# Optimization experiments

Measured on AMD Instinct MI355X. Metric: run time of the kernel, lower is better.

## Reference

```python
import jax, jax.numpy as jnp
import numpy as np

N_HEADS = 4

def log_cosh(x):
    # numerically stable log(cosh(x)) = |x| + log1p(exp(-2|x|)) - log(2)
    ax = jnp.abs(x)
    return ax + jnp.log1p(jnp.exp(-2.0 * ax)) - jnp.log(2.0)

def setup_inputs() -> dict:
    key = jax.random.key(0)
    ks = jax.random.split(key, 7)
    B, I, A, E, H = 4, 2048, 2048, 256, N_HEADS
    return {
        "query": jax.random.normal(ks[0], (B, I, E), dtype=jnp.float32),
        "key": jax.random.normal(ks[1], (B, A, E), dtype=jnp.float32),
        "value": jax.random.normal(ks[2], (B, A, E), dtype=jnp.float32),
        "distances": jax.random.uniform(ks[3], (B, I, A), dtype=jnp.float32),
        "in_proj_w": jax.random.normal(ks[4], (3 * E, E), dtype=jnp.float32) * 0.05,
        "out_proj_w": jax.random.normal(ks[5], (E, E), dtype=jnp.float32) * 0.05,
        "mass_w": jax.random.normal(ks[6], (H, E), dtype=jnp.float32) * 0.05,
    }

def reference(query, key, value, distances, in_proj_w, out_proj_w, mass_w):
    B, I, E = query.shape
    A = key.shape[1]
    H = N_HEADS
    D = E // H
    # distance-decay additive bias: mass is (B, A, H), nonnegative via log_cosh
    mass = log_cosh(key @ mass_w.T)                       # (B, A, H)
    bias = jnp.einsum('bah,bia->bhia', -mass, distances)  # (B, H, I, A)
    # nn.MultiheadAttention (bias=False) projections
    wq, wk, wv = jnp.split(in_proj_w, 3, axis=0)          # each (E, E)
    q = (query @ wq.T).reshape(B, I, H, D).transpose(0, 2, 1, 3)  # (B,H,I,D)
    k = (key @ wk.T).reshape(B, A, H, D).transpose(0, 2, 1, 3)    # (B,H,A,D)
    v = (value @ wv.T).reshape(B, A, H, D).transpose(0, 2, 1, 3)  # (B,H,A,D)
    scale = 1.0 / jnp.sqrt(jnp.asarray(D, dtype=q.dtype))
    scores = jnp.einsum('bhid,bhad->bhia', q, k) * scale + bias
    attn = jax.nn.softmax(scores, axis=-1)
    o = jnp.einsum('bhia,bhad->bhid', attn, v)            # (B,H,I,D)
    o = o.transpose(0, 2, 1, 3).reshape(B, I, E)
    return o @ out_proj_w.T
```

## Files before the change

kernel.cpp:

```cpp
#include <hip/hip_runtime.h>
#include <hip/hip_bf16.h>
#include <math.h>

#define BB 4
#define II 2048
#define AA 2048
#define EE 256
#define HH 4

typedef __bf16 bf16_t;
typedef bf16_t bf16x8 __attribute__((ext_vector_type(8)));
typedef bf16_t bf16x4 __attribute__((ext_vector_type(4)));
typedef float  f32x4  __attribute__((ext_vector_type(4)));

static __device__ __forceinline__ f32x4 mfma16(bf16x8 a, bf16x8 b, f32x4 c) {
    return __builtin_amdgcn_mfma_f32_16x16x32_bf16(a, b, c, 0, 0, 0);
}

__global__ __launch_bounds__(256) void mass_kernel(
    const float* __restrict__ key, const float* __restrict__ mass_w,
    float* __restrict__ massT)
{
    const int w = threadIdx.x >> 6;
    const int l = threadIdx.x & 63;
    const int row = blockIdx.x * 4 + w;
    f32x4 kv = *(const f32x4*)(key + (size_t)row * EE + l * 4);
    const int b = row >> 11, a = row & (AA - 1);
    #pragma unroll
    for (int h = 0; h < HH; ++h) {
        f32x4 mw = *(const f32x4*)(mass_w + h * EE + l * 4);
        float s = kv[0]*mw[0] + kv[1]*mw[1] + kv[2]*mw[2] + kv[3]*mw[3];
        #pragma unroll
        for (int off = 32; off >= 1; off >>= 1) s += __shfl_xor(s, off, 64);
        if (l == 0) {
            float ax = fabsf(s);
            massT[((size_t)b * HH + h) * AA + a] =
                ax + log1pf(__expf(-2.0f * ax)) - 0.693147180559945f;
        }
    }
}

template<int TRANS>
__global__ __launch_bounds__(256) void proj_gemm(
    const float* __restrict__ Aop, const float* __restrict__ Bop,
    bf16_t* __restrict__ Cout)
{
    __shared__ __align__(16) bf16_t sA[64][72];
    __shared__ __align__(16) bf16_t sB[64][72];
    const int t = threadIdx.x;
    const int w = t >> 6, l = t & 63, g = l >> 4, q = l & 15;
    const int wm = w >> 1, wn = w & 1;
    const int m0 = blockIdx.x * 64, n0 = blockIdx.y * 64;
    const int r = t >> 2, s = t & 3;

    f32x4 acc[2][2] = {};

    for (int kt = 0; kt < 4; ++kt) {
        {
            const float* ga = Aop + (size_t)(m0 + r) * EE + kt * 64 + s * 16;
            float tmp[16];
            *(f32x4*)&tmp[0]  = *(const f32x4*)(ga + 0);
            *(f32x4*)&tmp[4]  = *(const f32x4*)(ga + 4);
            *(f32x4*)&tmp[8]  = *(const f32x4*)(ga + 8);
            *(f32x4*)&tmp[12] = *(const f32x4*)(ga + 12);
            bf16x8 w0, w1;
            #pragma unroll
            for (int i = 0; i < 8; ++i) { w0[i] = (bf16_t)tmp[i]; w1[i] = (bf16_t)tmp[8 + i]; }
            *(bf16x8*)&sA[r][s * 16]     = w0;
            *(bf16x8*)&sA[r][s * 16 + 8] = w1;
        }
        {
            const float* gb = Bop + (size_t)(n0 + r) * EE + kt * 64 + s * 16;
            float tmp[16];
            *(f32x4*)&tmp[0]  = *(const f32x4*)(gb + 0);
            *(f32x4*)&tmp[4]  = *(const f32x4*)(gb + 4);
            *(f32x4*)&tmp[8]  = *(const f32x4*)(gb + 8);
            *(f32x4*)&tmp[12] = *(const f32x4*)(gb + 12);
            bf16x8 w0, w1;
            #pragma unroll
            for (int i = 0; i < 8; ++i) { w0[i] = (bf16_t)tmp[i]; w1[i] = (bf16_t)tmp[8 + i]; }
            *(bf16x8*)&sB[r][s * 16]     = w0;
            *(bf16x8*)&sB[r][s * 16 + 8] = w1;
        }
        __syncthreads();
        #pragma unroll
        for (int ks = 0; ks < 2; ++ks) {
            bf16x8 aA[2], aB[2];
            #pragma unroll
            for (int f = 0; f < 2; ++f) {
                aA[f] = *(const bf16x8*)&sA[wm * 32 + f * 16 + q][ks * 32 + g * 8];
                aB[f] = *(const bf16x8*)&sB[wn * 32 + f * 16 + q][ks * 32 + g * 8];
            }
            #pragma unroll
            for (int fm = 0; fm < 2; ++fm)
            #pragma unroll
            for (int fn = 0; fn < 2; ++fn)
                acc[fm][fn] = mfma16(aA[fm], aB[fn], acc[fm][fn]);
        }
        __syncthreads();
    }
    #pragma unroll
    for (int fm = 0; fm < 2; ++fm)
    #pragma unroll
    for (int fn = 0; fn < 2; ++fn)
    #pragma unroll
    for (int j = 0; j < 4; ++j) {
        const int m = m0 + wm * 32 + fm * 16 + g * 4 + j;
        const int n = n0 + wn * 32 + fn * 16 + q;
        const bf16_t v = (bf16_t)acc[fm][fn][j];
        if (TRANS == 0) {
            Cout[(size_t)m * EE + n] = v;
        } else {
            const int b = n >> 11, a = n & (AA - 1);
            Cout[(size_t)b * (AA * EE) + (size_t)(a >> 6) * (EE * 64) + m * 64 + (a & 63)] = v;
        }
    }
}

__global__ __launch_bounds__(256) void out_gemm(
    const bf16_t* __restrict__ Aop, const float* __restrict__ Bop,
    float* __restrict__ Cout)
{
    __shared__ __align__(16) bf16_t sA[64][72];
    __shared__ __align__(16) bf16_t sB[64][72];
    const int t = threadIdx.x;
    const int w = t >> 6, l = t & 63, g = l >> 4, q = l & 15;
    const int wm = w >> 1, wn = w & 1;
    const int m0 = blockIdx.x * 64, n0 = blockIdx.y * 64;
    const int r = t >> 2, s = t & 3;

    f32x4 acc[2][2] = {};

    for (int kt = 0; kt < 4; ++kt) {
        {
            const bf16_t* ga = Aop + (size_t)(m0 + r) * EE + kt * 64 + s * 16;
            *(bf16x8*)&sA[r][s * 16]     = *(const bf16x8*)(ga);
            *(bf16x8*)&sA[r][s * 16 + 8] = *(const bf16x8*)(ga + 8);
        }
        {
            const float* gb = Bop + (size_t)(n0 + r) * EE + kt * 64 + s * 16;
            float tmp[16];
            *(f32x4*)&tmp[0]  = *(const f32x4*)(gb + 0);
            *(f32x4*)&tmp[4]  = *(const f32x4*)(gb + 4);
            *(f32x4*)&tmp[8]  = *(const f32x4*)(gb + 8);
            *(f32x4*)&tmp[12] = *(const f32x4*)(gb + 12);
            bf16x8 w0, w1;
            #pragma unroll
            for (int i = 0; i < 8; ++i) { w0[i] = (bf16_t)tmp[i]; w1[i] = (bf16_t)tmp[8 + i]; }
            *(bf16x8*)&sB[r][s * 16]     = w0;
            *(bf16x8*)&sB[r][s * 16 + 8] = w1;
        }
        __syncthreads();
        #pragma unroll
        for (int ks = 0; ks < 2; ++ks) {
            bf16x8 aA[2], aB[2];
            #pragma unroll
            for (int f = 0; f < 2; ++f) {
                aA[f] = *(const bf16x8*)&sA[wm * 32 + f * 16 + q][ks * 32 + g * 8];
                aB[f] = *(const bf16x8*)&sB[wn * 32 + f * 16 + q][ks * 32 + g * 8];
            }
            #pragma unroll
            for (int fm = 0; fm < 2; ++fm)
            #pragma unroll
            for (int fn = 0; fn < 2; ++fn)
                acc[fm][fn] = mfma16(aA[fm], aB[fn], acc[fm][fn]);
        }
        __syncthreads();
    }
    #pragma unroll
    for (int fm = 0; fm < 2; ++fm)
    #pragma unroll
    for (int fn = 0; fn < 2; ++fn)
    #pragma unroll
    for (int j = 0; j < 4; ++j) {
        const int m = m0 + wm * 32 + fm * 16 + g * 4 + j;
        const int n = n0 + wn * 32 + fn * 16 + q;
        Cout[(size_t)m * EE + n] = acc[fm][fn][j];
    }
}

__global__ __launch_bounds__(256, 2) void attn_kernel(
    const bf16_t* __restrict__ Qp, const bf16_t* __restrict__ Kp,
    const bf16_t* __restrict__ Vt, const float* __restrict__ massT,
    const float* __restrict__ dist, bf16_t* __restrict__ Obuf)
{
    __shared__ __align__(16) bf16_t sK[2][64 * 64];
    __shared__ __align__(16) bf16_t sV[2][64 * 64];
    __shared__ __align__(16) float  sD[2][64 * 68];
    __shared__ __align__(16) float  sM[AA];

    const int t = threadIdx.x;
    const int w = t >> 6, l = t & 63, g = l >> 4, q = l & 15;
    const int h = blockIdx.y, b = blockIdx.z;
    const int i0 = blockIdx.x * 64;

    {
        const float* gm = massT + ((size_t)b * HH + h) * AA + t * 8;
        *(f32x4*)&sM[t * 8]     = *(const f32x4*)(gm);
        *(f32x4*)&sM[t * 8 + 4] = *(const f32x4*)(gm + 4);
    }

    bf16x8 qf[2];
    #pragma unroll
    for (int ks = 0; ks < 2; ++ks)
        qf[ks] = *(const bf16x8*)(Qp + (size_t)(b * II + i0 + w * 16 + q) * EE
                                     + h * 64 + ks * 32 + g * 8);

    const int sr = t >> 2;
    const int sc = (t & 3) * 2;
    const int z0 = ((sc)     ^ (sr & 7)) * 8;
    const int z1 = ((sc + 1) ^ (sr & 7)) * 8;

    const bf16_t* gK = Kp + ((size_t)b * AA + sr) * EE + h * 64 + sc * 8;
    const bf16_t* gV = Vt + (size_t)b * (AA * EE) + (size_t)(h * 64 + sr) * 64 + sc * 8;
    const float*  gD = dist + ((size_t)b * II + i0 + sr) * AA + (t & 3) * 16;

    bf16x8 rk0, rk1, rv0, rv1;
    f32x4 rd0, rd1, rd2, rd3;

    auto load_regs = [&](int a0) {
        const bf16_t* pk = gK + (size_t)a0 * EE;
        rk0 = *(const bf16x8*)(pk);
        rk1 = *(const bf16x8*)(pk + 8);
        const bf16_t* pv = gV + (size_t)(a0 >> 6) * (EE * 64);
        rv0 = *(const bf16x8*)(pv);
        rv1 = *(const bf16x8*)(pv + 8);
        const float* pd = gD + a0;
        rd0 = *(const f32x4*)(pd);
        rd1 = *(const f32x4*)(pd + 4);
        rd2 = *(const f32x4*)(pd + 8);
        rd3 = *(const f32x4*)(pd + 12);
    };
    auto write_stage = [&](int buf) {
        *(bf16x8*)&sK[buf][sr * 64 + z0] = rk0;
        *(bf16x8*)&sK[buf][sr * 64 + z1] = rk1;
        *(bf16x8*)&sV[buf][sr * 64 + z0] = rv0;
        *(bf16x8*)&sV[buf][sr * 64 + z1] = rv1;
        float* pd = &sD[buf][sr * 68 + (t & 3) * 16];
        *(f32x4*)(pd)      = rd0;
        *(f32x4*)(pd + 4)  = rd1;
        *(f32x4*)(pd + 8)  = rd2;
        *(f32x4*)(pd + 12) = rd3;
    };

    float mrun = -INFINITY, lrun = 0.f;
    f32x4 oacc[4] = {};

    load_regs(0);
    write_stage(0);
    __syncthreads();

    for (int tt = 0; tt < 32; ++tt) {
        const int buf = tt & 1;
        const int a0 = tt * 64;
        if (tt < 31) load_regs(a0 + 64);

        f32x4 st[4] = {};
        __builtin_amdgcn_s_setprio(1);
        #pragma unroll
        for (int fa = 0; fa < 4; ++fa) {
            const int row = fa * 16 + q;
            #pragma unroll
            for (int ks = 0; ks < 2; ++ks) {
                bf16x8 ak = *(const bf16x8*)&sK[buf][row * 64 + (((ks * 4 + g) ^ (row & 7)) * 8)];
                st[fa] = mfma16(ak, qf[ks], st[fa]);
            }
        }
        __builtin_amdgcn_s_setprio(0);

        float mloc = -INFINITY;
        const int drow = w * 16 + q;
        #pragma unroll
        for (int fa = 0; fa < 4; ++fa) {
            f32x4 df = *(const f32x4*)&sD[buf][drow * 68 + fa * 16 + g * 4];
            f32x4 ms = *(const f32x4*)&sM[a0 + fa * 16 + g * 4];
            #pragma unroll
            for (int j = 0; j < 4; ++j) {
                float sv = st[fa][j] * 0.125f - ms[j] * df[j];
                st[fa][j] = sv;
                mloc = fmaxf(mloc, sv);
            }
        }
        mloc = fmaxf(mloc, __shfl_xor(mloc, 16, 64));
        mloc = fmaxf(mloc, __shfl_xor(mloc, 32, 64));

        const bool skip = __all(mloc <= mrun);
        float mnew, sc;
        if (skip) { mnew = mrun; sc = 1.f; }
        else { mnew = fmaxf(mrun, mloc); sc = __expf(mrun - mnew); mrun = mnew; }

        float rs = 0.f;
        #pragma unroll
        for (int fa = 0; fa < 4; ++fa)
        #pragma unroll
        for (int j = 0; j < 4; ++j) {
            float e = __expf(st[fa][j] - mnew);
            st[fa][j] = e;
            rs += e;
        }
        rs += __shfl_xor(rs, 16, 64);
        rs += __shfl_xor(rs, 32, 64);
        lrun = lrun * sc + rs;

        if (!skip) {
            float osc[4];
            #pragma unroll
            for (int j = 0; j < 4; ++j) osc[j] = __shfl(sc, g * 4 + j, 64);
            #pragma unroll
            for (int fd = 0; fd < 4; ++fd)
            #pragma unroll
            for (int j = 0; j < 4; ++j) oacc[fd][j] *= osc[j];
        }

        bf16x8 pa[2];
        #pragma unroll
        for (int ka = 0; ka < 2; ++ka)
        #pragma unroll
        for (int j = 0; j < 8; ++j)
            pa[ka][j] = (bf16_t)st[2 * ka + (j >> 2)][j & 3];

        __builtin_amdgcn_s_setprio(1);
        #pragma unroll
        for (int ka = 0; ka < 2; ++ka)
        #pragma unroll
        for (int fd = 0; fd < 4; ++fd) {
            const int row = fd * 16 + q;
            const int base = row * 64 + (g & 1) * 4;
            bf16x4 v0 = *(const bf16x4*)&sV[buf][base + (((ka * 4 +     (g >> 1)) ^ (row & 7)) * 8)];
            bf16x4 v1 = *(const bf16x4*)&sV[buf][base + (((ka * 4 + 2 + (g >> 1)) ^ (row & 7)) * 8)];
            bf16x8 bv;
            #pragma unroll
            for (int j = 0; j < 4; ++j) { bv[j] = v0[j]; bv[4 + j] = v1[j]; }
            oacc[fd] = mfma16(pa[ka], bv, oacc[fd]);
        }
        __builtin_amdgcn_s_setprio(0);

        if (tt < 31) write_stage(buf ^ 1);
        __syncthreads();
    }

    float inv[4];
    #pragma unroll
    for (int j = 0; j < 4; ++j) inv[j] = 1.0f / __shfl(lrun, g * 4 + j, 64);
    #pragma unroll
    for (int fd = 0; fd < 4; ++fd)
    #pragma unroll
    for (int j = 0; j < 4; ++j) {
        const int mrow = i0 + w * 16 + g * 4 + j;
        const int ncol = h * 64 + fd * 16 + q;
        Obuf[(size_t)(b * II + mrow) * EE + ncol] = (bf16_t)(oacc[fd][j] * inv[j]);
    }
}

extern "C" void kernel_launch(void* const* d_in, const int* in_sizes, int n_in,
                              void* d_out, int out_size, void* d_ws, size_t ws_size,
                              hipStream_t stream)
{
    const float* query  = (const float*)d_in[0];
    const float* key    = (const float*)d_in[1];
    const float* value  = (const float*)d_in[2];
    const float* dist   = (const float*)d_in[3];
    const float* in_w   = (const float*)d_in[4];
    const float* out_w  = (const float*)d_in[5];
    const float* mass_w = (const float*)d_in[6];
    float* out = (float*)d_out;

    char* ws = (char*)d_ws;
    bf16_t* Qp    = (bf16_t*)(ws);
    bf16_t* Kp    = (bf16_t*)(ws + 1 * 4194304);
    bf16_t* Vt    = (bf16_t*)(ws + 2 * 4194304);
    bf16_t* Obuf  = (bf16_t*)(ws + 3 * 4194304);
    float*  massT = (float*) (ws + 4 * 4194304);

    dim3 blk(256);
    proj_gemm<0><<<dim3(128, 4), blk, 0, stream>>>(query, in_w,           Qp);
    proj_gemm<0><<<dim3(128, 4), blk, 0, stream>>>(key,   in_w + 65536,   Kp);
    proj_gemm<1><<<dim3(4, 128), blk, 0, stream>>>(in_w + 131072, value,  Vt);
    mass_kernel<<<dim3(2048), blk, 0, stream>>>(key, mass_w, massT);
    attn_kernel<<<dim3(32, 4, 4), blk, 0, stream>>>(Qp, Kp, Vt, massT, dist, Obuf);
    out_gemm<<<dim3(128, 4), blk, 0, stream>>>(Obuf, out_w, out);
}
```

Before: 98.97 us.

## Fuse pre-projections and split attention KV across two wave groups with direct-to-LDS loads

Merges the Q/K/V projections and the mass kernel into one launch, indexed by blockIdx.z. The attention kernel moves to 512 threads, where two wave groups each handle alternating KV tiles. K and V tiles are staged with global_load_lds, and distances are read straight into registers instead of through LDS. The two partial softmax states are merged through shared memory at the end. The softmax is switched to exp2 with log2e folded into the scale and the mass, which adds a combine step and more registers per block.

```diff
diff --git a/kernel.cpp b/kernel.cpp
--- a/kernel.cpp
+++ b/kernel.cpp
@@ -8,6 +8,9 @@
 #define EE 256
 #define HH 4
 
+#define LOG2E 1.4426950408889634f
+#define SCL   (0.125f * LOG2E)
+
 typedef __bf16 bf16_t;
 typedef bf16_t bf16x8 __attribute__((ext_vector_type(8)));
 typedef bf16_t bf16x4 __attribute__((ext_vector_type(4)));
@@ -17,40 +20,20 @@
     return __builtin_amdgcn_mfma_f32_16x16x32_bf16(a, b, c, 0, 0, 0);
 }
 
-__global__ __launch_bounds__(256) void mass_kernel(
-    const float* __restrict__ key, const float* __restrict__ mass_w,
-    float* __restrict__ massT)
+static __device__ __forceinline__ void glds16(const bf16_t* g, const bf16_t* l) {
+    __builtin_amdgcn_global_load_lds(
+        (const __attribute__((address_space(1))) void*)g,
+        (__attribute__((address_space(3))) void*)l, 16, 0, 0);
+}
+
+static __device__ __forceinline__ void proj_body(
+    const float* __restrict__ Aop, const float* __restrict__ Bop,
+    bf16_t* __restrict__ Cout, int m0, int n0, int TRANS,
+    bf16_t (*sA)[72], bf16_t (*sB)[72])
 {
-    const int w = threadIdx.x >> 6;
-    const int l = threadIdx.x & 63;
-    const int row = blockIdx.x * 4 + w;
-    f32x4 kv = *(const f32x4*)(key + (size_t)row * EE + l * 4);
-    const int b = row >> 11, a = row & (AA - 1);
-    #pragma unroll
-    for (int h = 0; h < HH; ++h) {
-        f32x4 mw = *(const f32x4*)(mass_w + h * EE + l * 4);
-        float s = kv[0]*mw[0] + kv[1]*mw[1] + kv[2]*mw[2] + kv[3]*mw[3];
-        #pragma unroll
-        for (int off = 32; off >= 1; off >>= 1) s += __shfl_xor(s, off, 64);
-        if (l == 0) {
-            float ax = fabsf(s);
-            massT[((size_t)b * HH + h) * AA + a] =
-                ax + log1pf(__expf(-2.0f * ax)) - 0.693147180559945f;
-        }
-    }
-}
-
-template<int TRANS>
-__global__ __launch_bounds__(256) void proj_gemm(
-    const float* __restrict__ Aop, const float* __restrict__ Bop,
-    bf16_t* __restrict__ Cout)
-{
-    __shared__ __align__(16) bf16_t sA[64][72];
-    __shared__ __align__(16) bf16_t sB[64][72];
     const int t = threadIdx.x;
     const int w = t >> 6, l = t & 63, g = l >> 4, q = l & 15;
     const int wm = w >> 1, wn = w & 1;
-    const int m0 = blockIdx.x * 64, n0 = blockIdx.y * 64;
     const int r = t >> 2, s = t & 3;
 
     f32x4 acc[2][2] = {};
@@ -111,8 +94,49 @@
         if (TRANS == 0) {
             Cout[(size_t)m * EE + n] = v;
         } else {
-            const int b = n >> 11, a = n & (AA - 1);
-            Cout[(size_t)b * (AA * EE) + (size_t)(a >> 6) * (EE * 64) + m * 64 + (a & 63)] = v;
+            const int bb = n >> 11, a = n & (AA - 1);
+            Cout[(size_t)bb * (AA * EE) + (size_t)(a >> 6) * (EE * 64) + m * 64 + (a & 63)] = v;
+        }
+    }
+}
+
+__global__ __launch_bounds__(256) void fused_pre(
+    const float* __restrict__ query, const float* __restrict__ key,
+    const float* __restrict__ value, const float* __restrict__ in_w,
+    const float* __restrict__ mass_w,
+    bf16_t* __restrict__ Qp, bf16_t* __restrict__ Kp, bf16_t* __restrict__ Vt,
+    float* __restrict__ massT)
+{
+    __shared__ __align__(16) bf16_t sA[64][72];
+    __shared__ __align__(16) bf16_t sB[64][72];
+    const int z = blockIdx.z;
+    if (z == 0) {
+        proj_body(query, in_w, Qp, blockIdx.x * 64, blockIdx.y * 64, 0, sA, sB);
+    } else if (z == 1) {
+        proj_body(key, in_w + 65536, Kp, blockIdx.x * 64, blockIdx.y * 64, 0, sA, sB);
+    } else if (z == 2) {
+        proj_body(in_w + 131072, value, Vt, blockIdx.y * 64, blockIdx.x * 64, 1, sA, sB);
+    } else {
+        const int w = threadIdx.x >> 6, l = threadIdx.x & 63;
+        const int p = blockIdx.y * 128 + blockIdx.x;
+        const int row0 = p * 16 + w * 4;
+        #pragma unroll
+        for (int rr = 0; rr < 4; ++rr) {
+            const int row = row0 + rr;
+            f32x4 kv = *(const f32x4*)(key + (size_t)row * EE + l * 4);
+            const int bb = row >> 11, a = row & (AA - 1);
+            #pragma unroll
+            for (int hh = 0; hh < HH; ++hh) {
+                f32x4 mw = *(const f32x4*)(mass_w + hh * EE + l * 4);
+                float sdot = kv[0]*mw[0] + kv[1]*mw[1] + kv[2]*mw[2] + kv[3]*mw[3];
+                #pragma unroll
+                for (int off = 32; off >= 1; off >>= 1) sdot += __shfl_xor(sdot, off, 64);
+                if (l == 0) {
+                    float ax = fabsf(sdot);
+                    massT[((size_t)bb * HH + hh) * AA + a] =
+                        (ax + log1pf(__expf(-2.0f * ax)) - 0.693147180559945f) * LOG2E;
+                }
+            }
         }
     }
 }
@@ -179,81 +203,64 @@
     }
 }
 
-__global__ __launch_bounds__(256, 2) void attn_kernel(
+__global__ __launch_bounds__(512, 4) void attn_kernel(
     const bf16_t* __restrict__ Qp, const bf16_t* __restrict__ Kp,
     const bf16_t* __restrict__ Vt, const float* __restrict__ massT,
     const float* __restrict__ dist, bf16_t* __restrict__ Obuf)
 {
-    __shared__ __align__(16) bf16_t sK[2][64 * 64];
-    __shared__ __align__(16) bf16_t sV[2][64 * 64];
-    __shared__ __align__(16) float  sD[2][64 * 68];
-    __shared__ __align__(16) float  sM[AA];
+    __shared__ __align__(16) bf16_t sK[2][2][4096];
+    __shared__ __align__(16) bf16_t sV[2][2][4096];
+    __shared__ __align__(16) float  sM[2048];
 
     const int t = threadIdx.x;
-    const int w = t >> 6, l = t & 63, g = l >> 4, q = l & 15;
+    const int wv = t >> 6, l = t & 63, g = l >> 4, q = l & 15;
+    const int s = wv >> 2, rg = wv & 3;
     const int h = blockIdx.y, b = blockIdx.z;
     const int i0 = blockIdx.x * 64;
 
-    {
-        const float* gm = massT + ((size_t)b * HH + h) * AA + t * 8;
-        *(f32x4*)&sM[t * 8]     = *(const f32x4*)(gm);
-        *(f32x4*)&sM[t * 8 + 4] = *(const f32x4*)(gm + 4);
-    }
+    *(f32x4*)&sM[t * 4] = *(const f32x4*)(massT + ((size_t)b * HH + h) * AA + t * 4);
 
     bf16x8 qf[2];
     #pragma unroll
     for (int ks = 0; ks < 2; ++ks)
-        qf[ks] = *(const bf16x8*)(Qp + (size_t)(b * II + i0 + w * 16 + q) * EE
+        qf[ks] = *(const bf16x8*)(Qp + (size_t)(b * II + i0 + rg * 16 + q) * EE
                                      + h * 64 + ks * 32 + g * 8);
 
-    const int sr = t >> 2;
-    const int sc = (t & 3) * 2;
-    const int z0 = ((sc)     ^ (sr & 7)) * 8;
-    const int z1 = ((sc + 1) ^ (sr & 7)) * 8;
-
-    const bf16_t* gK = Kp + ((size_t)b * AA + sr) * EE + h * 64 + sc * 8;
-    const bf16_t* gV = Vt + (size_t)b * (AA * EE) + (size_t)(h * 64 + sr) * 64 + sc * 8;
-    const float*  gD = dist + ((size_t)b * II + i0 + sr) * AA + (t & 3) * 16;
-
-    bf16x8 rk0, rk1, rv0, rv1;
-    f32x4 rd0, rd1, rd2, rd3;
-
-    auto load_regs = [&](int a0) {
-        const bf16_t* pk = gK + (size_t)a0 * EE;
-        rk0 = *(const bf16x8*)(pk);
-        rk1 = *(const bf16x8*)(pk + 8);
-        const bf16_t* pv = gV + (size_t)(a0 >> 6) * (EE * 64);
-        rv0 = *(const bf16x8*)(pv);
-        rv1 = *(const bf16x8*)(pv + 8);
-        const float* pd = gD + a0;
-        rd0 = *(const f32x4*)(pd);
-        rd1 = *(const f32x4*)(pd + 4);
-        rd2 = *(const f32x4*)(pd + 8);
-        rd3 = *(const f32x4*)(pd + 12);
+    const int u0 = rg * 2;
+    const int drow0 = u0 * 8 + (l >> 3);
+    const int cc = l & 7;
+
+    auto stage = [&](int a0, int kb) {
+        #pragma unroll
+        for (int u = 0; u < 2; ++u) {
+            const int dr = drow0 + u * 8;
+            const int cs = cc ^ (dr & 7);
+            glds16(Kp + ((size_t)b * AA + a0 + dr) * EE + h * 64 + cs * 8,
+                   &sK[s][kb][(u0 + u) * 512]);
+            glds16(Vt + (size_t)b * (AA * EE) + (size_t)(a0 >> 6) * (EE * 64)
+                      + (size_t)(h * 64 + dr) * 64 + cs * 8,
+                   &sV[s][kb][(u0 + u) * 512]);
+        }
     };
-    auto write_stage = [&](int buf) {
-        *(bf16x8*)&sK[buf][sr * 64 + z0] = rk0;
-        *(bf16x8*)&sK[buf][sr * 64 + z1] = rk1;
-        *(bf16x8*)&sV[buf][sr * 64 + z0] = rv0;
-        *(bf16x8*)&sV[buf][sr * 64 + z1] = rv1;
-        float* pd = &sD[buf][sr * 68 + (t & 3) * 16];
-        *(f32x4*)(pd)      = rd0;
-        *(f32x4*)(pd + 4)  = rd1;
-        *(f32x4*)(pd + 8)  = rd2;
-        *(f32x4*)(pd + 12) = rd3;
+
+    f32x4 rd[4];
+    auto load_dist = [&](int a0) {
+        const float* gd = dist + ((size_t)b * II + i0 + rg * 16 + q) * AA + a0 + g * 4;
+        #pragma unroll
+        for (int fa = 0; fa < 4; ++fa) rd[fa] = *(const f32x4*)(gd + fa * 16);
     };
+
+    stage(s * 64, 0);
+    load_dist(s * 64);
+    __syncthreads();
 
     float mrun = -INFINITY, lrun = 0.f;
     f32x4 oacc[4] = {};
 
-    load_regs(0);
-    write_stage(0);
-    __syncthreads();
-
-    for (int tt = 0; tt < 32; ++tt) {
-        const int buf = tt & 1;
-        const int a0 = tt * 64;
-        if (tt < 31) load_regs(a0 + 64);
+    for (int k = 0; k < 16; ++k) {
+        const int kb = k & 1;
+        const int a0 = (2 * k + s) * 64;
+        if (k < 15) stage(a0 + 128, kb ^ 1);
 
         f32x4 st[4] = {};
         __builtin_amdgcn_s_setprio(1);
@@ -262,39 +269,38 @@
             const int row = fa * 16 + q;
             #pragma unroll
             for (int ks = 0; ks < 2; ++ks) {
-                bf16x8 ak = *(const bf16x8*)&sK[buf][row * 64 + (((ks * 4 + g) ^ (row & 7)) * 8)];
+                bf16x8 ak = *(const bf16x8*)&sK[s][kb][row * 64 + (((ks * 4 + g) ^ (row & 7)) * 8)];
                 st[fa] = mfma16(ak, qf[ks], st[fa]);
             }
         }
         __builtin_amdgcn_s_setprio(0);
 
         float mloc = -INFINITY;
-        const int drow = w * 16 + q;
         #pragma unroll
         for (int fa = 0; fa < 4; ++fa) {
-            f32x4 df = *(const f32x4*)&sD[buf][drow * 68 + fa * 16 + g * 4];
             f32x4 ms = *(const f32x4*)&sM[a0 + fa * 16 + g * 4];
             #pragma unroll
             for (int j = 0; j < 4; ++j) {
-                float sv = st[fa][j] * 0.125f - ms[j] * df[j];
+                float sv = st[fa][j] * SCL - ms[j] * rd[fa][j];
                 st[fa][j] = sv;
                 mloc = fmaxf(mloc, sv);
             }
         }
+        if (k < 15) load_dist(a0 + 128);
+
         mloc = fmaxf(mloc, __shfl_xor(mloc, 16, 64));
         mloc = fmaxf(mloc, __shfl_xor(mloc, 32, 64));
-
         const bool skip = __all(mloc <= mrun);
         float mnew, sc;
         if (skip) { mnew = mrun; sc = 1.f; }
-        else { mnew = fmaxf(mrun, mloc); sc = __expf(mrun - mnew); mrun = mnew; }
+        else { mnew = fmaxf(mrun, mloc); sc = exp2f(mrun - mnew); mrun = mnew; }
 
         float rs = 0.f;
         #pragma unroll
         for (int fa = 0; fa < 4; ++fa)
         #pragma unroll
         for (int j = 0; j < 4; ++j) {
-            float e = __expf(st[fa][j] - mnew);
+            float e = exp2f(st[fa][j] - mnew);
             st[fa][j] = e;
             rs += e;
         }
@@ -326,8 +332,8 @@
         for (int fd = 0; fd < 4; ++fd) {
             const int row = fd * 16 + q;
             const int base = row * 64 + (g & 1) * 4;
-            bf16x4 v0 = *(const bf16x4*)&sV[buf][base + (((ka * 4 +     (g >> 1)) ^ (row & 7)) * 8)];
-            bf16x4 v1 = *(const bf16x4*)&sV[buf][base + (((ka * 4 + 2 + (g >> 1)) ^ (row & 7)) * 8)];
+            bf16x4 v0 = *(const bf16x4*)&sV[s][kb][base + (((ka * 4 +     (g >> 1)) ^ (row & 7)) * 8)];
+            bf16x4 v1 = *(const bf16x4*)&sV[s][kb][base + (((ka * 4 + 2 + (g >> 1)) ^ (row & 7)) * 8)];
             bf16x8 bv;
             #pragma unroll
             for (int j = 0; j < 4; ++j) { bv[j] = v0[j]; bv[4 + j] = v1[j]; }
@@ -335,20 +341,40 @@
         }
         __builtin_amdgcn_s_setprio(0);
 
-        if (tt < 31) write_stage(buf ^ 1);
         __syncthreads();
     }
 
-    float inv[4];
-    #pragma unroll
-    for (int j = 0; j < 4; ++j) inv[j] = 1.0f / __shfl(lrun, g * 4 + j, 64);
-    #pragma unroll
-    for (int fd = 0; fd < 4; ++fd)
-    #pragma unroll
-    for (int j = 0; j < 4; ++j) {
-        const int mrow = i0 + w * 16 + g * 4 + j;
-        const int ncol = h * 64 + fd * 16 + q;
-        Obuf[(size_t)(b * II + mrow) * EE + ncol] = (bf16_t)(oacc[fd][j] * inv[j]);
+    float* cb = (float*)&sK[0][0][0];
+    if (s == 1) {
+        float* p = cb + (rg * 64 + l) * 20;
+        p[0] = mrun; p[1] = lrun;
+        #pragma unroll
+        for (int fd = 0; fd < 4; ++fd) *(f32x4*)(p + 2 + fd * 4) = oacc[fd];
+    }
+    __syncthreads();
+    if (s == 0) {
+        const float* p = cb + (rg * 64 + l) * 20;
+        const float mB = p[0], lB = p[1];
+        const float mS = fmaxf(mrun, mB);
+        const float aS = exp2f(mrun - mS), bS = exp2f(mB - mS);
+        const float lS = lrun * aS + lB * bS;
+        float aSo[4], bSo[4], inv[4];
+        #pragma unroll
+        for (int j = 0; j < 4; ++j) {
+            aSo[j] = __shfl(aS, g * 4 + j, 64);
+            bSo[j] = __shfl(bS, g * 4 + j, 64);
+            inv[j] = 1.0f / __shfl(lS, g * 4 + j, 64);
+        }
+        #pragma unroll
+        for (int fd = 0; fd < 4; ++fd) {
+            f32x4 ob = *(const f32x4*)(p + 2 + fd * 4);
+            #pragma unroll
+            for (int j = 0; j < 4; ++j) {
+                const float o = (oacc[fd][j] * aSo[j] + ob[j] * bSo[j]) * inv[j];
+                Obuf[(size_t)(b * II + i0 + rg * 16 + g * 4 + j) * EE
+                     + h * 64 + fd * 16 + q] = (bf16_t)o;
+            }
+        }
     }
 }
 
@@ -372,11 +398,8 @@
     bf16_t* Obuf  = (bf16_t*)(ws + 3 * 4194304);
     float*  massT = (float*) (ws + 4 * 4194304);
 
-    dim3 blk(256);
-    proj_gemm<0><<<dim3(128, 4), blk, 0, stream>>>(query, in_w,           Qp);
-    proj_gemm<0><<<dim3(128, 4), blk, 0, stream>>>(key,   in_w + 65536,   Kp);
-    proj_gemm<1><<<dim3(4, 128), blk, 0, stream>>>(in_w + 131072, value,  Vt);
-    mass_kernel<<<dim3(2048), blk, 0, stream>>>(key, mass_w, massT);
-    attn_kernel<<<dim3(32, 4, 4), blk, 0, stream>>>(Qp, Kp, Vt, massT, dist, Obuf);
-    out_gemm<<<dim3(128, 4), blk, 0, stream>>>(Obuf, out_w, out);
-}
+    fused_pre<<<dim3(128, 4, 4), dim3(256), 0, stream>>>(
+        query, key, value, in_w, mass_w, Qp, Kp, Vt, massT);
+    attn_kernel<<<dim3(32, 4, 4), dim3(512), 0, stream>>>(Qp, Kp, Vt, massT, dist, Obuf);
+    out_gemm<<<dim3(128, 4), dim3(256), 0, stream>>>(Obuf, out_w, out);
+}
```

After: 91.96 us. 1.08x faster.
